# Optimization experiments

Hardware: AMD Instinct MI355X
Metric: run time of the kernel (lower is better)

The kernel has to match this reference:

```python
import jax, jax.numpy as jnp
import numpy as np

B, D, H, W = 512, 32, 128, 128


def setup_inputs() -> dict:
    key = jax.random.key(0)
    k1, k2, k3, k4 = jax.random.split(key, 4)
    inputs = jax.random.uniform(k1, (B, D), dtype=jnp.float32)
    stamp = jax.random.uniform(k2, (H, W, 1), dtype=jnp.float32)
    rows = jax.random.randint(k3, (D,), 0, H)
    cols = jax.random.randint(k4, (D,), 0, W)
    coords = jnp.stack([rows, cols], axis=-1).astype(jnp.int32)  # [D,2]
    return {"inputs": inputs, "stamp": stamp, "coords": coords}


def _static_indices(d, h, w):
    # rows/cols replication counts (static, numpy)
    rows_per = np.full(d, h // d, np.int32); rows_per[: h % d] += 1
    cols_per = np.full(d, w // d, np.int32); cols_per[: w % d] += 1
    # equidistant bar layout
    bar_w = w // (3 * d + 2)
    total_gap = w - d * bar_w
    gap = total_gap // (d + 1)
    extra = total_gap - gap * (d + 1)
    beg = extra // 2
    col_to_bar = np.full(w, -1, np.int32)
    for i in range(d):
        s = beg + i * (bar_w + gap) + gap
        col_to_bar[s : s + bar_w] = i
    return rows_per, cols_per, col_to_bar


def reference(inputs, stamp, coords):
    b, d = inputs.shape
    h, w = stamp.shape[:2]
    rows_per, cols_per, col_to_bar = _static_indices(d, h, w)

    # channel 1: deepinsight scatter (duplicates sum, matching tf.scatter_nd)
    di = jnp.zeros((b, h, w), inputs.dtype).at[:, coords[:, 0], coords[:, 1]].add(inputs)

    # channel 2: row-wise copy
    row_idx = np.repeat(np.arange(d), rows_per)  # [h]
    rowcopy = jnp.broadcast_to(inputs[:, row_idx][:, :, None], (b, h, w))

    # channel 3: normalized pairwise abs distance, expanded to h x w
    dm = jnp.abs(inputs[:, :, None] - inputs[:, None, :])  # [b,d,d]
    mn = jnp.min(dm, axis=(1, 2), keepdims=True)
    mx = jnp.max(dm, axis=(1, 2), keepdims=True)
    nd = (dm - mn) / (mx - mn)
    nd = nd[:, np.repeat(np.arange(d), rows_per), :][:, :, np.repeat(np.arange(d), cols_per)]

    # channel 4: equidistant bar graph (bars fill rows [0, bar_height))
    bar_height = jnp.clip(jnp.round(inputs * h).astype(jnp.int32), 0, h)  # [b,d]
    mask = (jnp.arange(h)[None, :, None] < bar_height[:, None, :]).astype(inputs.dtype)  # [b,h,d]
    safe = np.where(col_to_bar < 0, 0, col_to_bar)
    bars = mask[:, :, safe] * (col_to_bar >= 0).astype(inputs.dtype)[None, None, :]  # [b,h,w]

    stamp_b = jnp.broadcast_to(stamp, (b, h, w, 1))
    return jnp.concatenate(
        [stamp_b, di[..., None], rowcopy[..., None], nd[..., None], bars[..., None]], axis=-1
    )
```

## Files before the change

kernel.cpp:

```cpp
#include <hip/hip_runtime.h>


__global__ __launch_bounds__(256) void di_main(const float* __restrict__ inputs,
                                               const float* __restrict__ stamp,
                                               const int* __restrict__ coords,
                                               float* __restrict__ out) {
    const int blk = blockIdx.x;
    const int b = blk >> 3;
    const int part = blk & 7;
    const int tid = threadIdx.x;
    const int lane = tid & 63;

    __shared__ float buf[2][256 * 20];

    const float v = inputs[b * 32 + (lane & 31)];
    int bt = (int)rintf(v * 128.0f);
    bt = bt < 0 ? 0 : (bt > 128 ? 128 : bt);
    float mn = v, mx = v;
#pragma unroll
    for (int off = 1; off < 32; off <<= 1) {
        mn = fminf(mn, __shfl_xor(mn, off));
        mx = fmaxf(mx, __shfl_xor(mx, off));
    }
    const float inv = 1.0f / (mx - mn);

    auto compute = [&](int c, float* vals) {
        const int lp = part * 2048 + c * 1024 + tid * 4;
        const int h = lp >> 7;
        const int w0 = lp & 127;
        const float rowv = __shfl(v, h >> 2);
        const float ndv = fabsf(rowv - __shfl(v, w0 >> 2)) * inv;
        const float4 sv = *reinterpret_cast<const float4*>(stamp + h * 128 + w0);
        const float svj[4] = {sv.x, sv.y, sv.z, sv.w};
#pragma unroll
        for (int j = 0; j < 4; ++j) {
            const int w = w0 + j;
            const int t = w - 17;
            const int bar = t / 3;
            const bool valid = (t >= 0) && (t <= 93) && (t - bar * 3 == 0);
            const int bhv = __shfl(bt, valid ? bar : 0);
            const float barv = (valid && h < bhv) ? 1.0f : 0.0f;
            vals[5 * j + 0] = svj[j];
            vals[5 * j + 1] = 0.0f;
            vals[5 * j + 2] = rowv;
            vals[5 * j + 3] = ndv;
            vals[5 * j + 4] = barv;
        }
    };
    auto stage = [&](int c, const float* vals) {
        float4* lw = reinterpret_cast<float4*>(&buf[c][tid * 20]);
        const float4* src = reinterpret_cast<const float4*>(vals);
#pragma unroll
        for (int k = 0; k < 5; ++k) lw[k] = src[k];
    };
    auto flush = [&](int c) {
        float4* dst = reinterpret_cast<float4*>(out) +
                      (size_t)b * 20480 + (size_t)part * 2560 + (size_t)c * 1280;
        const float4* lr = reinterpret_cast<const float4*>(buf[c]);
#pragma unroll
        for (int it = 0; it < 5; ++it) {
            const int f = it * 256 + tid;
            dst[f] = lr[f];
        }
    };

    alignas(16) float valsA[20], valsB[20];
    compute(0, valsA);
    stage(0, valsA);
    __syncthreads();
    compute(1, valsB);
    stage(1, valsB);
    flush(0);
    __syncthreads();
    flush(1);

    __syncthreads();
    if (tid < 32) {
        const int r = coords[2 * tid], c = coords[2 * tid + 1];
        if ((r >> 4) == part)
            atomicAdd(out + ((size_t)b * 16384 + (size_t)(r * 128 + c)) * 5 + 1,
                      __shfl(v, tid));
    }
}

extern "C" void kernel_launch(void* const* d_in, const int* in_sizes, int n_in,
                              void* d_out, int out_size, void* d_ws, size_t ws_size,
                              hipStream_t stream) {
    const float* inputs = (const float*)d_in[0];
    const float* stamp  = (const float*)d_in[1];
    const int*   coords = (const int*)d_in[2];
    float* out = (float*)d_out;

    di_main<<<4096, 256, 0, stream>>>(inputs, stamp, coords, out);
}
```

Measured before the change: 167.1 us.

## Fold scatter into shared tile before store and split blocks into smaller parts

Each block now covers 8 rows instead of 16, so the grid doubles. A single shared staging buffer replaces the double-buffered pair. The scatter of inputs into channel 1 is now done with shared-memory atomics on the staged tile before the coalesced flush, which removes the global atomic read-modify-write that used to follow the stores. An occupancy hint of 8 blocks per CU is added. The intent is more parallelism and no extra global traffic for the scatter, at the cost of losing the overlap between staging and flushing inside a block.

```diff
diff --git a/kernel.cpp b/kernel.cpp
--- a/kernel.cpp
+++ b/kernel.cpp
@@ -1,17 +1,17 @@
 #include <hip/hip_runtime.h>
 
 
-__global__ __launch_bounds__(256) void di_main(const float* __restrict__ inputs,
-                                               const float* __restrict__ stamp,
-                                               const int* __restrict__ coords,
-                                               float* __restrict__ out) {
-    const int blk = blockIdx.x;
-    const int b = blk >> 3;
-    const int part = blk & 7;
-    const int tid = threadIdx.x;
+__global__ __launch_bounds__(256, 8) void di_main(const float* __restrict__ inputs,
+                                                  const float* __restrict__ stamp,
+                                                  const int* __restrict__ coords,
+                                                  float* __restrict__ out) {
+    const int blk  = blockIdx.x;
+    const int b    = blk >> 4;
+    const int part = blk & 15;
+    const int tid  = threadIdx.x;
     const int lane = tid & 63;
 
-    __shared__ float buf[2][256 * 20];
+    __shared__ float buf[256 * 20];
 
     const float v = inputs[b * 32 + (lane & 31)];
     int bt = (int)rintf(v * 128.0f);
@@ -24,62 +24,52 @@
     }
     const float inv = 1.0f / (mx - mn);
 
-    auto compute = [&](int c, float* vals) {
-        const int lp = part * 2048 + c * 1024 + tid * 4;
-        const int h = lp >> 7;
-        const int w0 = lp & 127;
-        const float rowv = __shfl(v, h >> 2);
-        const float ndv = fabsf(rowv - __shfl(v, w0 >> 2)) * inv;
-        const float4 sv = *reinterpret_cast<const float4*>(stamp + h * 128 + w0);
-        const float svj[4] = {sv.x, sv.y, sv.z, sv.w};
+    const int lp = part * 1024 + tid * 4;
+    const int h  = lp >> 7;
+    const int w0 = lp & 127;
+    const float rowv = __shfl(v, h >> 2);
+    const float ndv  = fabsf(rowv - v) * inv;
+    const float4 sv  = *reinterpret_cast<const float4*>(stamp + lp);
+    const float svj[4] = {sv.x, sv.y, sv.z, sv.w};
+
+    alignas(16) float vals[20];
 #pragma unroll
-        for (int j = 0; j < 4; ++j) {
-            const int w = w0 + j;
-            const int t = w - 17;
-            const int bar = t / 3;
-            const bool valid = (t >= 0) && (t <= 93) && (t - bar * 3 == 0);
-            const int bhv = __shfl(bt, valid ? bar : 0);
-            const float barv = (valid && h < bhv) ? 1.0f : 0.0f;
-            vals[5 * j + 0] = svj[j];
-            vals[5 * j + 1] = 0.0f;
-            vals[5 * j + 2] = rowv;
-            vals[5 * j + 3] = ndv;
-            vals[5 * j + 4] = barv;
-        }
-    };
-    auto stage = [&](int c, const float* vals) {
-        float4* lw = reinterpret_cast<float4*>(&buf[c][tid * 20]);
+    for (int j = 0; j < 4; ++j) {
+        const int w = w0 + j;
+        const int t = w - 17;
+        const int bar = t / 3;
+        const bool valid = (t >= 0) && (t <= 93) && (t - bar * 3 == 0);
+        const int bhv = __shfl(bt, valid ? bar : 0);
+        vals[5 * j + 0] = svj[j];
+        vals[5 * j + 1] = 0.0f;
+        vals[5 * j + 2] = rowv;
+        vals[5 * j + 3] = ndv;
+        vals[5 * j + 4] = (valid && h < bhv) ? 1.0f : 0.0f;
+    }
+    {
+        float4* lw = reinterpret_cast<float4*>(&buf[tid * 20]);
         const float4* src = reinterpret_cast<const float4*>(vals);
 #pragma unroll
         for (int k = 0; k < 5; ++k) lw[k] = src[k];
-    };
-    auto flush = [&](int c) {
-        float4* dst = reinterpret_cast<float4*>(out) +
-                      (size_t)b * 20480 + (size_t)part * 2560 + (size_t)c * 1280;
-        const float4* lr = reinterpret_cast<const float4*>(buf[c]);
+    }
+    __syncthreads();
+
+    if (tid < 32) {
+        const int2 rc = reinterpret_cast<const int2*>(coords)[tid];
+        if ((rc.x >> 3) == part) {
+            const int pp = rc.x * 128 + rc.y - part * 1024;
+            atomicAdd(&buf[(pp >> 2) * 20 + (pp & 3) * 5 + 1], v);
+        }
+    }
+    __syncthreads();
+
+    float4* dst = reinterpret_cast<float4*>(out) +
+                  (size_t)b * 20480 + (size_t)part * 1280;
+    const float4* lr = reinterpret_cast<const float4*>(buf);
 #pragma unroll
-        for (int it = 0; it < 5; ++it) {
-            const int f = it * 256 + tid;
-            dst[f] = lr[f];
-        }
-    };
-
-    alignas(16) float valsA[20], valsB[20];
-    compute(0, valsA);
-    stage(0, valsA);
-    __syncthreads();
-    compute(1, valsB);
-    stage(1, valsB);
-    flush(0);
-    __syncthreads();
-    flush(1);
-
-    __syncthreads();
-    if (tid < 32) {
-        const int r = coords[2 * tid], c = coords[2 * tid + 1];
-        if ((r >> 4) == part)
-            atomicAdd(out + ((size_t)b * 16384 + (size_t)(r * 128 + c)) * 5 + 1,
-                      __shfl(v, tid));
+    for (int it = 0; it < 5; ++it) {
+        const int f = it * 256 + tid;
+        dst[f] = lr[f];
     }
 }
 
@@ -91,5 +81,5 @@
     const int*   coords = (const int*)d_in[2];
     float* out = (float*)d_out;
 
-    di_main<<<4096, 256, 0, stream>>>(inputs, stamp, coords, out);
+    di_main<<<8192, 256, 0, stream>>>(inputs, stamp, coords, out);
 }
```

Result: no change. 166.3 us, median of 2 (-0.5%).
